# Kernel optimization log

Hardware: AMD Instinct MI355X
Metric: run time of the kernel (lower is better)

The kernel has to match this reference:

```python
import jax, jax.numpy as jnp
import numpy as np

B, T, D, H = 32, 1024, 512, 256  # batch, seq_len, input_size, lstm hidden per direction (2H == D)


def _lstm_dir(x_tbd, W_ih, W_hh, b):
    """Single-direction LSTM over time-major input [T, B, D] -> hidden states [T, B, H].
    PyTorch gate order: i, f, g, o."""
    xg = jnp.einsum('tbd,gd->tbg', x_tbd, W_ih) + b  # precompute input projections [T,B,4H]
    h0 = jnp.zeros((x_tbd.shape[1], W_hh.shape[1]), x_tbd.dtype)

    def step(carry, xt):
        h, c = carry
        g = xt + h @ W_hh.T
        i, f, gg, o = jnp.split(g, 4, axis=-1)
        c = jax.nn.sigmoid(f) * c + jax.nn.sigmoid(i) * jnp.tanh(gg)
        h = jax.nn.sigmoid(o) * jnp.tanh(c)
        return (h, c), h

    _, hs = jax.lax.scan(step, (h0, h0), xg)
    return hs


def setup_inputs() -> dict:
    key = jax.random.key(0)
    ks = jax.random.split(key, 10)
    s = 0.05
    # padding mask: 1 (True) for padding positions, built from random valid lengths
    lengths = jax.random.randint(ks[1], (B,), T // 2, T)
    x_mask = jnp.arange(T)[None, :] >= lengths[:, None]  # bool [B, T]
    return {
        'x': jax.random.normal(ks[0], (B, T, D), jnp.float32),
        'x_mask': x_mask,
        'W_ih_f': jax.random.normal(ks[2], (4 * H, D), jnp.float32) * s,
        'W_hh_f': jax.random.normal(ks[3], (4 * H, H), jnp.float32) * s,
        'b_f': jnp.zeros((4 * H,), jnp.float32),
        'W_ih_b': jax.random.normal(ks[4], (4 * H, D), jnp.float32) * s,
        'W_hh_b': jax.random.normal(ks[5], (4 * H, H), jnp.float32) * s,
        'b_b': jnp.zeros((4 * H,), jnp.float32),
        'W_l': jax.random.normal(ks[6], (D, D), jnp.float32) * s,
    }


def reference(x, x_mask, W_ih_f, W_hh_f, b_f, W_ih_b, W_hh_b, b_b, W_l):
    # BiRNN encode: 1-layer bidirectional LSTM, concat directions -> [B, T, 2H] == [B, T, D]
    xt = jnp.swapaxes(x, 0, 1)  # [T, B, D]
    h_f = _lstm_dir(xt, W_ih_f, W_hh_f, b_f)
    h_b = _lstm_dir(xt[::-1], W_ih_b, W_hh_b, b_b)[::-1]
    xe = jnp.swapaxes(jnp.concatenate([h_f, h_b], axis=-1), 0, 1)  # [B, T, D]

    # Bilinear self-attention: L = (x W_l^T) x^T, mask padded query rows, softmax, weighted sum
    proj = xe @ W_l.T  # [B, T, D]
    L = jnp.einsum('bid,bjd->bij', proj, xe)  # [B, T, T]
    L = jnp.where(x_mask[:, :, None], jnp.float32(-1e30), L)
    A = jax.nn.softmax(L, axis=-1)
    return jnp.einsum('bij,bjd->bid', A, xe)  # [B, T, D]
```

## Files before the change

### kernel.cpp

```cpp
#include <hip/hip_runtime.h>
#include <math.h>

#define T_SEQ 1024
#define B_SZ  32
#define D_SZ  512
#define H_SZ  256

typedef unsigned short u16;
typedef short v8bf __attribute__((ext_vector_type(8)));
typedef float v4f  __attribute__((ext_vector_type(4)));

__device__ __forceinline__ unsigned int f2bf(float f)
{
    unsigned int u = __float_as_uint(f);
    return (u + 0x7fffu + ((u >> 16) & 1u)) >> 16;
}
__device__ __forceinline__ u16 f2bfu(float f)
{
    unsigned int u = __float_as_uint(f);
    return (u16)((u + 0x7fffu + ((u >> 16) & 1u)) >> 16);
}
__device__ __forceinline__ float bfu2f(u16 h)
{
    return __uint_as_float(((unsigned int)h) << 16);
}

__device__ __forceinline__ void gload_lds16(const void* g, void* l)
{
    __builtin_amdgcn_global_load_lds(
        (const __attribute__((address_space(1))) void*)g,
        (__attribute__((address_space(3))) void*)l,
        16, 0, 0);
}

#define BM 64
#define BN 64
#define BK 16

__global__ __launch_bounds__(256)
void gemm_nt(const float* __restrict__ A, const float* __restrict__ W,
             const float* __restrict__ bias, float* __restrict__ C,
             int M, int N, int K,
             long long sA, long long sW, long long sC)
{
    int z = blockIdx.z;
    A += (size_t)z * sA; W += (size_t)z * sW; C += (size_t)z * sC;
    int n0 = blockIdx.x * BN;
    int m0 = blockIdx.y * BM;
    int tid = threadIdx.x;
    int tm = tid >> 4, tn = tid & 15;

    __shared__ float As[BK][BM + 4];
    __shared__ float Ws[BK][BN + 4];

    float acc[4][4] = {};

    int lc = tid & 15;
    int lr = tid >> 4;

    for (int k0 = 0; k0 < K; k0 += BK) {
        #pragma unroll
        for (int i = 0; i < 4; ++i) {
            int r = lr + 16 * i;
            As[lc][r] = A[(size_t)(m0 + r) * K + k0 + lc];
            Ws[lc][r] = W[(size_t)(n0 + r) * K + k0 + lc];
        }
        __syncthreads();
        #pragma unroll
        for (int kk = 0; kk < BK; ++kk) {
            float4 a4 = *(const float4*)&As[kk][tm * 4];
            float4 b4 = *(const float4*)&Ws[kk][tn * 4];
            float a[4] = {a4.x, a4.y, a4.z, a4.w};
            float b[4] = {b4.x, b4.y, b4.z, b4.w};
            #pragma unroll
            for (int i = 0; i < 4; ++i)
                #pragma unroll
                for (int j = 0; j < 4; ++j)
                    acc[i][j] = fmaf(a[i], b[j], acc[i][j]);
        }
        __syncthreads();
    }

    float bb[4] = {0.f, 0.f, 0.f, 0.f};
    if (bias) {
        #pragma unroll
        for (int j = 0; j < 4; ++j) bb[j] = bias[n0 + tn * 4 + j];
    }
    #pragma unroll
    for (int i = 0; i < 4; ++i) {
        int m = m0 + tm * 4 + i;
        float4 o;
        o.x = acc[i][0] + bb[0];
        o.y = acc[i][1] + bb[1];
        o.z = acc[i][2] + bb[2];
        o.w = acc[i][3] + bb[3];
        *(float4*)&C[(size_t)m * N + n0 + tn * 4] = o;
    }
}

__global__ __launch_bounds__(256)
void gemm_nn(const float* __restrict__ A, const float* __restrict__ B,
             float* __restrict__ C, int M, int N, int K,
             long long sA, long long sB, long long sC)
{
    int z = blockIdx.z;
    A += (size_t)z * sA; B += (size_t)z * sB; C += (size_t)z * sC;
    int n0 = blockIdx.x * BN;
    int m0 = blockIdx.y * BM;
    int tid = threadIdx.x;
    int tm = tid >> 4, tn = tid & 15;

    __shared__ float As[BK][BM + 4];
    __shared__ float Bs[BK][BN + 4];

    float acc[4][4] = {};

    int lc = tid & 15;
    int lr = tid >> 4;
    int br = tid >> 6;
    int bc = tid & 63;

    for (int k0 = 0; k0 < K; k0 += BK) {
        #pragma unroll
        for (int i = 0; i < 4; ++i) {
            int r = lr + 16 * i;
            As[lc][r] = A[(size_t)(m0 + r) * K + k0 + lc];
        }
        #pragma unroll
        for (int i = 0; i < 4; ++i) {
            int r = br + 4 * i;
            Bs[r][bc] = B[(size_t)(k0 + r) * N + n0 + bc];
        }
        __syncthreads();
        #pragma unroll
        for (int kk = 0; kk < BK; ++kk) {
            float4 a4 = *(const float4*)&As[kk][tm * 4];
            float4 b4 = *(const float4*)&Bs[kk][tn * 4];
            float a[4] = {a4.x, a4.y, a4.z, a4.w};
            float b[4] = {b4.x, b4.y, b4.z, b4.w};
            #pragma unroll
            for (int i = 0; i < 4; ++i)
                #pragma unroll
                for (int j = 0; j < 4; ++j)
                    acc[i][j] = fmaf(a[i], b[j], acc[i][j]);
        }
        __syncthreads();
    }
    #pragma unroll
    for (int i = 0; i < 4; ++i) {
        int m = m0 + tm * 4 + i;
        float4 o;
        o.x = acc[i][0]; o.y = acc[i][1]; o.z = acc[i][2]; o.w = acc[i][3];
        *(float4*)&C[(size_t)m * N + n0 + tn * 4] = o;
    }
}

template<int EPI>
__global__ __launch_bounds__(256)
void gemm_ms(const u16* __restrict__ Ah, const u16* __restrict__ Al,
             const u16* __restrict__ Bh, const u16* __restrict__ Bl,
             const float* __restrict__ bias,
             float* __restrict__ C, u16* __restrict__ Chi, u16* __restrict__ Clo,
             int M, int N, int K,
             long long sA, long long sB, long long sC)
{
    int z = blockIdx.z;
    Ah += (size_t)z * sA; Al += (size_t)z * sA;
    Bh += (size_t)z * sB; Bl += (size_t)z * sB;
    int n0 = blockIdx.x * 128;
    int m0 = blockIdx.y * 128;
    int t  = threadIdx.x;
    int lane = t & 63, wid = t >> 6;

    __shared__ u16 sA_h[128 * 32];
    __shared__ u16 sA_l[128 * 32];
    __shared__ u16 sB_h[128 * 32];
    __shared__ u16 sB_l[128 * 32];

    int wm = (wid & 1) << 6;
    int wn = (wid >> 1) << 6;
    int fr = lane & 15;
    int g  = lane >> 4;

    v4f acc[4][4];
    #pragma unroll
    for (int i = 0; i < 4; ++i)
        #pragma unroll
        for (int j = 0; j < 4; ++j)
            acc[i][j] = (v4f){0.f, 0.f, 0.f, 0.f};

    int s0 = t;
    int s1 = t + 256;
    int r0 = s0 >> 2, gl0 = (s0 & 3) ^ ((s0 >> 3) & 3);
    int r1 = s1 >> 2, gl1 = (s1 & 3) ^ ((s1 >> 3) & 3);
    int lb0 = (wid << 6) << 3;
    int lb1 = ((wid << 6) + 256) << 3;

    for (int k0 = 0; k0 < K; k0 += 32) {
        size_t gA0 = (size_t)(m0 + r0) * K + k0 + gl0 * 8;
        size_t gA1 = (size_t)(m0 + r1) * K + k0 + gl1 * 8;
        size_t gB0 = (size_t)(n0 + r0) * K + k0 + gl0 * 8;
        size_t gB1 = (size_t)(n0 + r1) * K + k0 + gl1 * 8;
        gload_lds16(Ah + gA0, sA_h + lb0);
        gload_lds16(Ah + gA1, sA_h + lb1);
        gload_lds16(Al + gA0, sA_l + lb0);
        gload_lds16(Al + gA1, sA_l + lb1);
        gload_lds16(Bh + gB0, sB_h + lb0);
        gload_lds16(Bh + gB1, sB_h + lb1);
        gload_lds16(Bl + gB0, sB_l + lb0);
        gload_lds16(Bl + gB1, sB_l + lb1);
        __syncthreads();

        v8bf bhf[4], blf[4];
        #pragma unroll
        for (int ni = 0; ni < 4; ++ni) {
            int r = wn + ni * 16 + fr;
            int off = r * 32 + ((g ^ ((r >> 1) & 3)) << 3);
            bhf[ni] = *(const v8bf*)&sB_h[off];
            blf[ni] = *(const v8bf*)&sB_l[off];
        }
        #pragma unroll
        for (int mi = 0; mi < 4; ++mi) {
            int r = wm + mi * 16 + fr;
            int off = r * 32 + ((g ^ ((r >> 1) & 3)) << 3);
            v8bf ah = *(const v8bf*)&sA_h[off];
            v8bf al = *(const v8bf*)&sA_l[off];
            #pragma unroll
            for (int ni = 0; ni < 4; ++ni) {
                acc[mi][ni] = __builtin_amdgcn_mfma_f32_16x16x32_bf16(ah, bhf[ni], acc[mi][ni], 0, 0, 0);
                acc[mi][ni] = __builtin_amdgcn_mfma_f32_16x16x32_bf16(al, bhf[ni], acc[mi][ni], 0, 0, 0);
                acc[mi][ni] = __builtin_amdgcn_mfma_f32_16x16x32_bf16(ah, blf[ni], acc[mi][ni], 0, 0, 0);
            }
        }
        __syncthreads();
    }

    int ocol = lane & 15;
    int orow = (lane >> 4) << 2;
    if (EPI == 1) {
        #pragma unroll
        for (int mi = 0; mi < 4; ++mi) {
            #pragma unroll
            for (int rr = 0; rr < 4; ++rr) {
                int m = m0 + wm + mi * 16 + orow + rr;
                #pragma unroll
                for (int ni = 0; ni < 4; ++ni) {
                    int n = n0 + wn + ni * 16 + ocol;
                    float v = acc[mi][ni][rr];
                    u16 h = f2bfu(v);
                    Chi[(size_t)m * N + n] = h;
                    Clo[(size_t)m * N + n] = f2bfu(v - bfu2f(h));
                }
            }
        }
    } else {
        float* Cz = C + (size_t)z * sC;
        float bb[4] = {0.f, 0.f, 0.f, 0.f};
        if (bias) {
            #pragma unroll
            for (int ni = 0; ni < 4; ++ni) bb[ni] = bias[n0 + wn + ni * 16 + ocol];
        }
        #pragma unroll
        for (int mi = 0; mi < 4; ++mi) {
            #pragma unroll
            for (int rr = 0; rr < 4; ++rr) {
                int m = m0 + wm + mi * 16 + orow + rr;
                #pragma unroll
                for (int ni = 0; ni < 4; ++ni) {
                    int n = n0 + wn + ni * 16 + ocol;
                    Cz[(size_t)m * N + n] = acc[mi][ni][rr] + bb[ni];
                }
            }
        }
    }
}

__global__ __launch_bounds__(256)
void convert_split(const float4* __restrict__ in,
                   ushort4* __restrict__ hi, ushort4* __restrict__ lo)
{
    size_t i = (size_t)blockIdx.x * 256 + threadIdx.x;
    float4 v = in[i];
    ushort4 h, l;
    h.x = f2bfu(v.x); l.x = f2bfu(v.x - bfu2f(h.x));
    h.y = f2bfu(v.y); l.y = f2bfu(v.y - bfu2f(h.y));
    h.z = f2bfu(v.z); l.z = f2bfu(v.z - bfu2f(h.z));
    h.w = f2bfu(v.w); l.w = f2bfu(v.w - bfu2f(h.w));
    hi[i] = h;
    lo[i] = l;
}

__global__ __launch_bounds__(256)
void transpose_split_xe(const float* __restrict__ xe,
                        u16* __restrict__ Th, u16* __restrict__ Tl)
{
    int b = blockIdx.z;
    const float* X = xe + (size_t)b * T_SEQ * D_SZ;
    u16* TH = Th + (size_t)b * T_SEQ * D_SZ;
    u16* TL = Tl + (size_t)b * T_SEQ * D_SZ;
    int t0 = blockIdx.x << 5, d0 = blockIdx.y << 5;

    __shared__ float tile[32][33];
    int tx = threadIdx.x & 31, ty = threadIdx.x >> 5;

    #pragma unroll
    for (int i = 0; i < 4; ++i)
        tile[ty + (i << 3)][tx] = X[(size_t)(t0 + ty + (i << 3)) * D_SZ + d0 + tx];
    __syncthreads();
    #pragma unroll
    for (int i = 0; i < 4; ++i) {
        int dd = ty + (i << 3);
        float v = tile[tx][dd];
        u16 h = f2bfu(v);
        TH[(size_t)(d0 + dd) * T_SEQ + t0 + tx] = h;
        TL[(size_t)(d0 + dd) * T_SEQ + t0 + tx] = f2bfu(v - bfu2f(h));
    }
}

__global__ __launch_bounds__(256)
void pack_whh_bf16(const float* __restrict__ Wf, const float* __restrict__ Wb,
                   uint4* __restrict__ Wpf, uint4* __restrict__ Wpb)
{
    int idx = blockIdx.x * 256 + threadIdx.x;
    int u = idx & (H_SZ - 1);
    int p = idx >> 8;
    uint4 a, b;
    unsigned int* pa = (unsigned int*)&a;
    unsigned int* pb = (unsigned int*)&b;
    #pragma unroll
    for (int g = 0; g < 4; ++g) {
        size_t row = (size_t)(g * H_SZ + u) * H_SZ;
        pa[g] = f2bf(Wf[row + 2 * p]) | (f2bf(Wf[row + 2 * p + 1]) << 16);
        pb[g] = f2bf(Wb[row + 2 * p]) | (f2bf(Wb[row + 2 * p + 1]) << 16);
    }
    Wpf[idx] = a;
    Wpb[idx] = b;
}

__global__ __launch_bounds__(1024)
void lstm_bf16(const float* __restrict__ xgA, const uint4* __restrict__ WpA,
               const float* __restrict__ xgB, const uint4* __restrict__ WpB,
               float* __restrict__ xe, int d0, int fused)
{
    int i = blockIdx.x;
    int b, dir;
    if (fused) {
        int j = i & 7, m = i >> 3;
        dir = j >> 2;
        b   = (j & 3) * 8 + m;
    } else {
        b   = (i & 3) * 8 + (i >> 2);
        dir = d0;
    }
    const float* xg = dir ? xgB : xgA;
    const uint4* Wp = dir ? WpB : WpA;

    int tid   = threadIdx.x;
    int u     = tid & (H_SZ - 1);
    int slice = tid >> 8;
    int p0    = slice << 5;

    __shared__ float  hs[H_SZ];
    __shared__ float4 part[4][H_SZ];

    uint4 wres[16];
    {
        const uint4* wb = Wp + (size_t)p0 * H_SZ + u;
        #pragma unroll
        for (int q = 0; q < 16; ++q) wres[q] = wb[q * H_SZ];
    }
    const uint4* wstream = Wp + (size_t)(p0 + 16) * H_SZ + u;

    if (tid < H_SZ) hs[tid] = 0.f;
    float c = 0.f;
    __syncthreads();

    for (int s = 0; s < T_SEQ; ++s) {
        int t = dir ? (T_SEQ - 1 - s) : s;

        float xi = 0.f, xf = 0.f, xgv = 0.f, xo = 0.f;
        if (tid < H_SZ) {
            const float* row = xg + ((size_t)b * T_SEQ + t) * (4 * H_SZ);
            xi  = row[u];
            xf  = row[H_SZ + u];
            xgv = row[2 * H_SZ + u];
            xo  = row[3 * H_SZ + u];
        }

        float4 acc; acc.x = 0.f; acc.y = 0.f; acc.z = 0.f; acc.w = 0.f;

        #define DOT_PAIR(WQ, P)                                             \
        {                                                                   \
            float2 hp = *(const float2*)&hs[2 * (P)];                       \
            const unsigned int* wc = (const unsigned int*)&(WQ);            \
            _Pragma("unroll")                                               \
            for (int g = 0; g < 4; ++g) {                                   \
                float wlo = __uint_as_float(wc[g] << 16);                   \
                float whi = __uint_as_float(wc[g] & 0xffff0000u);           \
                ((float*)&acc)[g] =                                         \
                    fmaf(whi, hp.y, fmaf(wlo, hp.x, ((float*)&acc)[g]));    \
            }                                                               \
        }

        #pragma unroll
        for (int q = 0; q < 16; ++q) {
            DOT_PAIR(wres[q], p0 + q);
        }
        #pragma unroll
        for (int q = 0; q < 16; ++q) {
            int qr = (q + s) & 15;
            uint4 wq = wstream[(size_t)qr * H_SZ];
            DOT_PAIR(wq, p0 + 16 + qr);
        }
        #undef DOT_PAIR

        part[slice][u] = acc;
        __syncthreads();

        if (tid < H_SZ) {
            float4 pp0 = part[0][u], pp1 = part[1][u], pp2 = part[2][u], pp3 = part[3][u];
            float ai = xi  + pp0.x + pp1.x + pp2.x + pp3.x;
            float af = xf  + pp0.y + pp1.y + pp2.y + pp3.y;
            float ag = xgv + pp0.z + pp1.z + pp2.z + pp3.z;
            float ao = xo  + pp0.w + pp1.w + pp2.w + pp3.w;
            float ig = 1.f / (1.f + __expf(-ai));
            float fg = 1.f / (1.f + __expf(-af));
            float gg = tanhf(ag);
            float og = 1.f / (1.f + __expf(-ao));
            c = fg * c + ig * gg;
            float h = og * tanhf(c);
            hs[u] = h;
            xe[((size_t)b * T_SEQ + t) * D_SZ + dir * H_SZ + u] = h;
        }
        __syncthreads();
    }
}

__global__ __launch_bounds__(256)
void softmax_rows(float* __restrict__ L, const void* __restrict__ maskraw)
{
    const unsigned char* mu8 = (const unsigned char*)maskraw;
    const int*           mi32 = (const int*)maskraw;
    bool layout_u8 = (mu8[1023] != 0);

    int lane = threadIdx.x & 63;
    int wid  = threadIdx.x >> 6;
    int row  = (blockIdx.x << 2) + wid;
    float* p = L + (size_t)row * T_SEQ;

    int mval = layout_u8 ? (int)mu8[row] : mi32[row];

    if (mval != 0) {
        const float inv = 1.0f / (float)T_SEQ;
        for (int j = lane; j < T_SEQ; j += 64) p[j] = inv;
        return;
    }

    float v[16];
    float m = -1e30f;
    #pragma unroll
    for (int u = 0; u < 16; ++u) {
        v[u] = p[lane + (u << 6)];
        m = fmaxf(m, v[u]);
    }
    #pragma unroll
    for (int s = 32; s; s >>= 1) m = fmaxf(m, __shfl_xor(m, s, 64));

    float sum = 0.f;
    #pragma unroll
    for (int u = 0; u < 16; ++u) {
        v[u] = __expf(v[u] - m);
        sum += v[u];
    }
    #pragma unroll
    for (int s = 32; s; s >>= 1) sum += __shfl_xor(sum, s, 64);

    float inv = 1.0f / sum;
    #pragma unroll
    for (int u = 0; u < 16; ++u) p[lane + (u << 6)] = v[u] * inv;
}

extern "C" void kernel_launch(void* const* d_in, const int* in_sizes, int n_in,
                              void* d_out, int out_size, void* d_ws, size_t ws_size,
                              hipStream_t stream)
{
    const float* x     = (const float*)d_in[0];
    const void*  xmask = d_in[1];
    const float* Wih_f = (const float*)d_in[2];
    const float* Whh_f = (const float*)d_in[3];
    const float* b_f   = (const float*)d_in[4];
    const float* Wih_b = (const float*)d_in[5];
    const float* Whh_b = (const float*)d_in[6];
    const float* b_b   = (const float*)d_in[7];
    const float* W_l   = (const float*)d_in[8];
    float* out = (float*)d_out;

    char* ws = (char*)d_ws;
    const size_t MB1 = (size_t)1 << 20;
    const size_t SZ_XE = (size_t)B_SZ * T_SEQ * D_SZ * sizeof(float);
    const size_t SZ_XG = (size_t)B_SZ * T_SEQ * 4 * H_SZ * sizeof(float);
    bool fused = ws_size >= SZ_XE + 2 * SZ_XG;

    const int MT = B_SZ * T_SEQ;
    const long long sTD = (long long)T_SEQ * D_SZ;
    const long long sTT = (long long)T_SEQ * T_SEQ;

    uint4* Wpf = (uint4*)d_out;
    uint4* Wpb = (uint4*)d_out + 128 * H_SZ;

    pack_whh_bf16<<<dim3((128 * H_SZ) / 256), dim3(256), 0, stream>>>(
        Whh_f, Whh_b, Wpf, Wpb);

    if (fused) {
        u16* x_hi  = (u16*)(ws);
        u16* x_lo  = (u16*)(ws + 32 * MB1);
        float* xg_f = (float*)(ws + 64 * MB1);
        float* xg_b = (float*)(ws + 192 * MB1);
        float* xe   = (float*)(ws);
        u16* xe_hi = (u16*)(ws + 64 * MB1);
        u16* xe_lo = (u16*)(ws + 96 * MB1);
        u16* pj_hi = (u16*)(ws + 128 * MB1);
        u16* pj_lo = (u16*)(ws + 160 * MB1);
        float* L   = (float*)(ws + 192 * MB1);
        u16* xT_hi = pj_hi;
        u16* xT_lo = pj_lo;
        u16* L_hi  = (u16*)(ws);
        u16* L_lo  = (u16*)(ws + 64 * MB1);

        u16* Wihf_hi = (u16*)((char*)d_out + 1 * MB1);
        u16* Wihf_lo = (u16*)((char*)d_out + 2 * MB1);
        u16* Wihb_hi = (u16*)((char*)d_out + 3 * MB1);
        u16* Wihb_lo = (u16*)((char*)d_out + 4 * MB1);
        u16* Wl_hi   = (u16*)((char*)d_out + 5 * MB1);
        u16* Wl_lo   = (u16*)((char*)d_out + 5 * MB1 + (MB1 >> 1));

        convert_split<<<dim3((MT * D_SZ) / 1024), dim3(256), 0, stream>>>(
            (const float4*)x, (ushort4*)x_hi, (ushort4*)x_lo);
        convert_split<<<dim3((4 * H_SZ * D_SZ) / 1024), dim3(256), 0, stream>>>(
            (const float4*)Wih_f, (ushort4*)Wihf_hi, (ushort4*)Wihf_lo);
        convert_split<<<dim3((4 * H_SZ * D_SZ) / 1024), dim3(256), 0, stream>>>(
            (const float4*)Wih_b, (ushort4*)Wihb_hi, (ushort4*)Wihb_lo);
        convert_split<<<dim3((D_SZ * D_SZ) / 1024), dim3(256), 0, stream>>>(
            (const float4*)W_l, (ushort4*)Wl_hi, (ushort4*)Wl_lo);

        gemm_ms<0><<<dim3((4 * H_SZ) / 128, MT / 128, 1), dim3(256), 0, stream>>>(
            x_hi, x_lo, Wihf_hi, Wihf_lo, b_f, xg_f, nullptr, nullptr,
            MT, 4 * H_SZ, D_SZ, 0, 0, 0);
        gemm_ms<0><<<dim3((4 * H_SZ) / 128, MT / 128, 1), dim3(256), 0, stream>>>(
            x_hi, x_lo, Wihb_hi, Wihb_lo, b_b, xg_b, nullptr, nullptr,
            MT, 4 * H_SZ, D_SZ, 0, 0, 0);

        lstm_bf16<<<dim3(2 * B_SZ), dim3(1024), 0, stream>>>(
            xg_f, Wpf, xg_b, Wpb, xe, 0, 1);

        convert_split<<<dim3((MT * D_SZ) / 1024), dim3(256), 0, stream>>>(
            (const float4*)xe, (ushort4*)xe_hi, (ushort4*)xe_lo);

        gemm_ms<1><<<dim3(D_SZ / 128, MT / 128, 1), dim3(256), 0, stream>>>(
            xe_hi, xe_lo, Wl_hi, Wl_lo, nullptr, nullptr, pj_hi, pj_lo,
            MT, D_SZ, D_SZ, 0, 0, 0);

        gemm_ms<0><<<dim3(T_SEQ / 128, T_SEQ / 128, B_SZ), dim3(256), 0, stream>>>(
            pj_hi, pj_lo, xe_hi, xe_lo, nullptr, L, nullptr, nullptr,
            T_SEQ, T_SEQ, D_SZ, sTD, sTD, sTT);

        softmax_rows<<<dim3(MT / 4), dim3(256), 0, stream>>>(L, xmask);

        transpose_split_xe<<<dim3(T_SEQ / 32, D_SZ / 32, B_SZ), dim3(256), 0, stream>>>(
            xe, xT_hi, xT_lo);

        convert_split<<<dim3((MT * T_SEQ) / 1024), dim3(256), 0, stream>>>(
            (const float4*)L, (ushort4*)L_hi, (ushort4*)L_lo);

        gemm_ms<0><<<dim3(D_SZ / 128, T_SEQ / 128, B_SZ), dim3(256), 0, stream>>>(
            L_hi, L_lo, xT_hi, xT_lo, nullptr, out, nullptr, nullptr,
            T_SEQ, D_SZ, T_SEQ, sTT, sTD, sTD);
    } else {
        float* xe   = (float*)(ws);
        float* xg_f = (float*)(ws + SZ_XE);
        float* xg_b = xg_f;
        float* L    = xg_f;
        float* proj = out;

        gemm_nt<<<dim3((4 * H_SZ) / BN, MT / BM, 1), dim3(256), 0, stream>>>(
            x, Wih_f, b_f, xg_f, MT, 4 * H_SZ, D_SZ, 0, 0, 0);
        lstm_bf16<<<dim3(B_SZ), dim3(1024), 0, stream>>>(
            xg_f, Wpf, xg_f, Wpf, xe, 0, 0);
        gemm_nt<<<dim3((4 * H_SZ) / BN, MT / BM, 1), dim3(256), 0, stream>>>(
            x, Wih_b, b_b, xg_b, MT, 4 * H_SZ, D_SZ, 0, 0, 0);
        lstm_bf16<<<dim3(B_SZ), dim3(1024), 0, stream>>>(
            xg_b, Wpb, xg_b, Wpb, xe, 1, 0);

        gemm_nt<<<dim3(D_SZ / BN, MT / BM, 1), dim3(256), 0, stream>>>(
            xe, W_l, nullptr, proj, MT, D_SZ, D_SZ, 0, 0, 0);
        gemm_nt<<<dim3(T_SEQ / BN, T_SEQ / BM, B_SZ), dim3(256), 0, stream>>>(
            proj, xe, nullptr, L, T_SEQ, T_SEQ, D_SZ, sTD, sTD, sTT);
        softmax_rows<<<dim3(MT / 4), dim3(256), 0, stream>>>(L, xmask);
        gemm_nn<<<dim3(D_SZ / BN, T_SEQ / BM, B_SZ), dim3(256), 0, stream>>>(
            L, xe, out, T_SEQ, D_SZ, T_SEQ, sTT, sTD, sTD);
    }
}
```

Baseline: 17.09 ms.

## Prefetch streamed LSTM weights, use fast tanh, restructure split-bf16 MFMA loop

In the LSTM recurrence, streamed bf16 weight chunks are now loaded into an 8-deep register prefetch ring, so global load latency overlaps the dot-product FMAs. tanhf is replaced by an exp-based tanh with clamping to shorten the serial gate computation. The split-bf16 GEMM inner loop is reordered into three passes (hi*hi, lo*hi, hi*lo) so fewer fragments are live at once, and the LSTM kernel gets a min-blocks launch bound. The prefetch ring and launch bound raise register pressure in a 1024-thread block, and the fast tanh changes rounding slightly.

```diff
diff --git a/kernel.cpp b/kernel.cpp
--- a/kernel.cpp
+++ b/kernel.cpp
@@ -31,6 +31,13 @@
         (const __attribute__((address_space(1))) void*)g,
         (__attribute__((address_space(3))) void*)l,
         16, 0, 0);
+}
+
+__device__ __forceinline__ float tanh_fast(float x)
+{
+    float xc = fminf(fmaxf(x, -30.f), 30.f);
+    float e = __expf(-2.f * xc);
+    return (1.f - e) / (1.f + e);
 }
 
 #define BM 64
@@ -211,25 +218,24 @@
         gload_lds16(Bl + gB1, sB_l + lb1);
         __syncthreads();
 
-        v8bf bhf[4], blf[4];
-        #pragma unroll
-        for (int ni = 0; ni < 4; ++ni) {
-            int r = wn + ni * 16 + fr;
-            int off = r * 32 + ((g ^ ((r >> 1) & 3)) << 3);
-            bhf[ni] = *(const v8bf*)&sB_h[off];
-            blf[ni] = *(const v8bf*)&sB_l[off];
-        }
-        #pragma unroll
-        for (int mi = 0; mi < 4; ++mi) {
-            int r = wm + mi * 16 + fr;
-            int off = r * 32 + ((g ^ ((r >> 1) & 3)) << 3);
-            v8bf ah = *(const v8bf*)&sA_h[off];
-            v8bf al = *(const v8bf*)&sA_l[off];
+        #pragma unroll
+        for (int pass = 0; pass < 3; ++pass) {
+            const u16* sB_p = (pass == 2) ? sB_l : sB_h;
+            const u16* sA_p = (pass == 1) ? sA_l : sA_h;
+            v8bf bf[4];
             #pragma unroll
             for (int ni = 0; ni < 4; ++ni) {
-                acc[mi][ni] = __builtin_amdgcn_mfma_f32_16x16x32_bf16(ah, bhf[ni], acc[mi][ni], 0, 0, 0);
-                acc[mi][ni] = __builtin_amdgcn_mfma_f32_16x16x32_bf16(al, bhf[ni], acc[mi][ni], 0, 0, 0);
-                acc[mi][ni] = __builtin_amdgcn_mfma_f32_16x16x32_bf16(ah, blf[ni], acc[mi][ni], 0, 0, 0);
+                int r = wn + ni * 16 + fr;
+                bf[ni] = *(const v8bf*)&sB_p[r * 32 + ((g ^ ((r >> 1) & 3)) << 3)];
+            }
+            #pragma unroll
+            for (int mi = 0; mi < 4; ++mi) {
+                int r = wm + mi * 16 + fr;
+                v8bf af = *(const v8bf*)&sA_p[r * 32 + ((g ^ ((r >> 1) & 3)) << 3)];
+                #pragma unroll
+                for (int ni = 0; ni < 4; ++ni)
+                    acc[mi][ni] = __builtin_amdgcn_mfma_f32_16x16x32_bf16(
+                        af, bf[ni], acc[mi][ni], 0, 0, 0);
             }
         }
         __syncthreads();
@@ -337,7 +343,7 @@
     Wpb[idx] = b;
 }
 
-__global__ __launch_bounds__(1024)
+__global__ __launch_bounds__(1024, 4)
 void lstm_bf16(const float* __restrict__ xgA, const uint4* __restrict__ WpA,
                const float* __restrict__ xgB, const uint4* __restrict__ WpB,
                float* __restrict__ xe, int d0, int fused)
@@ -386,6 +392,11 @@
             xgv = row[2 * H_SZ + u];
             xo  = row[3 * H_SZ + u];
         }
+
+        uint4 pf[8];
+        #pragma unroll
+        for (int q = 0; q < 8; ++q)
+            pf[q] = wstream[(size_t)((q + s) & 15) * H_SZ];
 
         float4 acc; acc.x = 0.f; acc.y = 0.f; acc.z = 0.f; acc.w = 0.f;
 
@@ -408,8 +419,10 @@
         }
         #pragma unroll
         for (int q = 0; q < 16; ++q) {
+            uint4 wq = pf[q & 7];
+            if (q < 8)
+                pf[q & 7] = wstream[(size_t)((q + 8 + s) & 15) * H_SZ];
             int qr = (q + s) & 15;
-            uint4 wq = wstream[(size_t)qr * H_SZ];
             DOT_PAIR(wq, p0 + 16 + qr);
         }
         #undef DOT_PAIR
@@ -425,10 +438,10 @@
             float ao = xo  + pp0.w + pp1.w + pp2.w + pp3.w;
             float ig = 1.f / (1.f + __expf(-ai));
             float fg = 1.f / (1.f + __expf(-af));
-            float gg = tanhf(ag);
+            float gg = tanh_fast(ag);
             float og = 1.f / (1.f + __expf(-ao));
             c = fg * c + ig * gg;
-            float h = og * tanhf(c);
+            float h = og * tanh_fast(c);
             hs[u] = h;
             xe[((size_t)b * T_SEQ + t) * D_SZ + dir * H_SZ + u] = h;
         }
```

Result: slower. 17.58 ms (+2.8%).
